# Kernel tuning notes

Hardware: AMD Instinct MI355X
Metric: run time of the kernel (lower is better)

Reference implementation:

```python
import jax, jax.numpy as jnp
import numpy as np

B, S, HID, NH = 2, 2048, 1024, 16
HD = HID // NH
BASE = 10000.0


def _rope_tables(seq_len, head_dim):
    i = jnp.arange(0, head_dim, 2, dtype=jnp.float32)
    theta = BASE ** (-i / head_dim)
    pos = jnp.arange(seq_len, dtype=jnp.float32)
    m_theta = jnp.outer(pos, theta)  # [S, HD/2]
    cos = jnp.repeat(jnp.cos(m_theta), 2, axis=1)  # [S, HD]
    sin = jnp.repeat(jnp.sin(m_theta), 2, axis=1)
    return cos, sin


def _apply_rope(x, cos, sin):
    # x: [B, NH, S, HD]; interleaved rotation: (-x1, x0, -x3, x2, ...)
    x_even = x[..., 0::2]
    x_odd = x[..., 1::2]
    inv_x = jnp.stack((-x_odd, x_even), axis=-1).reshape(x.shape)
    return x * cos[None, None] + inv_x * sin[None, None]


def setup_inputs() -> dict:
    key = jax.random.key(0)
    ks = jax.random.split(key, 7)
    q = jax.random.normal(ks[0], (B, S, HID), dtype=jnp.float32)
    k = jax.random.normal(ks[1], (B, S, HID), dtype=jnp.float32)
    v = jax.random.normal(ks[2], (B, S, HID), dtype=jnp.float32)
    scale = 1.0 / np.sqrt(HID)
    Wq = jax.random.normal(ks[3], (HID, HID), dtype=jnp.float32) * scale
    Wk = jax.random.normal(ks[4], (HID, HID), dtype=jnp.float32) * scale
    Wv = jax.random.normal(ks[5], (HID, HID), dtype=jnp.float32) * scale
    Wo = jax.random.normal(ks[6], (HID, HID), dtype=jnp.float32) * scale
    mask = jnp.triu(jnp.ones((S, S), dtype=bool), k=1)[None, None]  # causal, True = masked
    return {"q": q, "k": k, "v": v, "mask": mask,
            "Wq": Wq, "Wk": Wk, "Wv": Wv, "Wo": Wo}


def reference(q, k, v, mask, Wq, Wk, Wv, Wo):
    cos, sin = _rope_tables(S, HD)
    # Linear (torch stores weight as [out, in]; y = x @ W.T)
    qh = (q @ Wq.T).reshape(B, S, NH, HD).transpose(0, 2, 1, 3)
    kh = (k @ Wk.T).reshape(B, S, NH, HD).transpose(0, 2, 1, 3)
    vh = (v @ Wv.T).reshape(B, S, NH, HD).transpose(0, 2, 1, 3)
    qh = _apply_rope(qh, cos, sin)
    kh = _apply_rope(kh, cos, sin)
    scores = jnp.einsum("bhqd,bhkd->bhqk", qh, kh) / np.sqrt(HD)
    neg_min = jnp.finfo(jnp.float32).min
    scores = jnp.where(mask, neg_min, scores)
    attn = jax.nn.softmax(scores, axis=-1)
    out = jnp.einsum("bhqk,bhkd->bhqd", attn, vh)  # [B,NH,S,HD]
    out = out.transpose(0, 2, 1, 3).reshape(B, S, HID)
    return out @ Wo.T
```

## Files before the change

kernel.cpp:

```cpp
#include <hip/hip_runtime.h>

#define S_LEN 2048
#define HIDN  1024
#define NHEAD 16
#define HDIM  64
#define MROWS 4096
#define KDIM  1024
#define NDIM  1024

typedef __attribute__((ext_vector_type(8))) short bf16x8;
typedef __attribute__((ext_vector_type(4))) float f32x4;

static __device__ __forceinline__ ushort f2bf(float f) {
    unsigned int u = __float_as_uint(f);
    u = (u + 0x7fffu + ((u >> 16) & 1u)) >> 16;
    return (ushort)u;
}

static __device__ __forceinline__ void gload16(const ushort* g, ushort* l) {
    __builtin_amdgcn_global_load_lds(
        (const __attribute__((address_space(1))) unsigned int*)g,
        (__attribute__((address_space(3))) unsigned int*)l, 16, 0, 0);
}

__global__ __launch_bounds__(256) void prep_kernel(
    const float* __restrict__ q, const float* __restrict__ k,
    const float* __restrict__ v, const float* __restrict__ Wq,
    const float* __restrict__ Wk, const float* __restrict__ Wv,
    const float* __restrict__ Wo,
    ushort* __restrict__ qb, ushort* __restrict__ kb, ushort* __restrict__ vb,
    ushort* __restrict__ Wqb, ushort* __restrict__ Wkb, ushort* __restrict__ Wvb,
    ushort* __restrict__ Wob,
    float* __restrict__ rc, float* __restrict__ rs)
{
    const long Q4 = (long)MROWS * KDIM / 4;
    const long W4 = (long)NDIM * KDIM / 4;
    if (blockIdx.x < 16384) {
        long i = (long)blockIdx.x * 256 + threadIdx.x;
        const float* src; ushort* dst; long off;
        if (i < Q4)          { src = q; dst = qb; off = i; }
        else if (i < 2 * Q4) { src = k; dst = kb; off = i - Q4; }
        else if (i < 3 * Q4) { src = v; dst = vb; off = i - 2 * Q4; }
        else {
            long t = i - 3 * Q4;
            int wsel = (int)(t >> 18);
            off = t & (W4 - 1);
            src = (wsel == 0) ? Wq : (wsel == 1) ? Wk : (wsel == 2) ? Wv : Wo;
            dst = (wsel == 0) ? Wqb : (wsel == 1) ? Wkb : (wsel == 2) ? Wvb : Wob;
        }
        float4 vv = ((const float4*)src)[off];
        ushort4 o;
        o.x = f2bf(vv.x); o.y = f2bf(vv.y); o.z = f2bf(vv.z); o.w = f2bf(vv.w);
        ((ushort4*)dst)[off] = o;
    } else {
        int idx = (blockIdx.x - 16384) * 256 + threadIdx.x;
        int s  = idx >> 5;
        int jp = idx & 31;
        float theta = expf(-(float)(2 * jp) * (9.210340371976184f / 64.0f));
        float ang = (float)s * theta;
        float sv, cv;
        sincosf(ang, &sv, &cv);
        rc[idx] = cv;
        rs[idx] = sv;
    }
}

static __device__ __forceinline__ void gemm_mainloop(
    const ushort* __restrict__ A, const ushort* __restrict__ W,
    ushort* As, ushort* Bs, f32x4 (&acc)[4][4], bool swapops,
    int m0, int n0, int tid)
{
    const int lane = tid & 63, wid = tid >> 6;
    const int wm = wid & 1, wn = wid >> 1;
    const int quad = lane >> 4, l15 = lane & 15;

    for (int k0 = 0; k0 < KDIM; k0 += 32) {
        __syncthreads();
#pragma unroll
        for (int rr = 0; rr < 2; ++rr) {
            int sidx = tid + rr * 256;
            int row = sidx >> 2;
            int g = (sidx & 3) ^ (row & 3);
            gload16(A + (size_t)(m0 + row) * KDIM + k0 + g * 8, As + sidx * 8);
            gload16(W + (size_t)(n0 + row) * KDIM + k0 + g * 8, Bs + sidx * 8);
        }
        __syncthreads();

        bf16x8 af[4], bfr[4];
#pragma unroll
        for (int i = 0; i < 4; ++i) {
            int row = wm * 64 + i * 16 + l15;
            int p = quad ^ (row & 3);
            af[i] = swapops ? *(const bf16x8*)&Bs[row * 32 + p * 8]
                            : *(const bf16x8*)&As[row * 32 + p * 8];
        }
#pragma unroll
        for (int j = 0; j < 4; ++j) {
            int row = wn * 64 + j * 16 + l15;
            int p = quad ^ (row & 3);
            bfr[j] = swapops ? *(const bf16x8*)&As[row * 32 + p * 8]
                             : *(const bf16x8*)&Bs[row * 32 + p * 8];
        }
#pragma unroll
        for (int i = 0; i < 4; ++i)
#pragma unroll
            for (int j = 0; j < 4; ++j)
                acc[i][j] = __builtin_amdgcn_mfma_f32_16x16x32_bf16(af[i], bfr[j],
                                                                    acc[i][j], 0, 0, 0);
    }
}

__global__ __launch_bounds__(256) void gemm_qkv(
    const ushort* __restrict__ qb, const ushort* __restrict__ kb,
    const ushort* __restrict__ vb,
    const ushort* __restrict__ Wqb, const ushort* __restrict__ Wkb,
    const ushort* __restrict__ Wvb,
    ushort* __restrict__ Qh, ushort* __restrict__ Kh, ushort* __restrict__ Vt,
    const float* __restrict__ rc, const float* __restrict__ rs)
{
    __shared__ __align__(16) ushort As[128 * 32];
    __shared__ __align__(16) ushort Bs[128 * 32];

    const int tid = threadIdx.x;
    const int lane = tid & 63, wid = tid >> 6;
    const int wm = wid & 1, wn = wid >> 1;
    const int quad = lane >> 4, l15 = lane & 15;
    const int m0 = blockIdx.y * 128, n0 = blockIdx.x * 128;
    const int z = blockIdx.z;

    const ushort* A = (z == 0) ? qb : (z == 1) ? kb : vb;
    const ushort* W = (z == 0) ? Wqb : (z == 1) ? Wkb : Wvb;

    f32x4 acc[4][4];
#pragma unroll
    for (int i = 0; i < 4; ++i)
#pragma unroll
        for (int j = 0; j < 4; ++j) acc[i][j] = 0.0f;

    gemm_mainloop(A, W, As, Bs, acc, (z == 2), m0, n0, tid);

    if (z != 2) {
        ushort* out = (z == 0) ? Qh : Kh;
        const float scale = (z == 0) ? 0.18033688011112042f : 1.0f;
#pragma unroll
        for (int i = 0; i < 4; ++i)
#pragma unroll
            for (int j = 0; j < 4; ++j)
#pragma unroll
                for (int r = 0; r < 4; ++r) {
                    int m = m0 + wm * 64 + i * 16 + quad * 4 + r;
                    int n = n0 + wn * 64 + j * 16 + l15;
                    float v = acc[i][j][r];
                    int b = m >> 11, s = m & (S_LEN - 1);
                    int h = n >> 6, d = n & 63;
                    int pidx = s * 32 + (d >> 1);
                    float cv = rc[pidx], sv = rs[pidx];
                    float partner = __shfl_xor(v, 1);
                    v = (d & 1) ? (v * cv + partner * sv)
                                : (v * cv - partner * sv);
                    out[((size_t)((b * NHEAD + h) * S_LEN + s)) * HDIM + d] =
                        f2bf(v * scale);
                }
    } else {
#pragma unroll
        for (int i = 0; i < 4; ++i)
#pragma unroll
            for (int j = 0; j < 4; ++j)
#pragma unroll
                for (int r = 0; r < 4; ++r) {
                    int nrow = n0 + wm * 64 + i * 16 + quad * 4 + r;
                    int mcol = m0 + wn * 64 + j * 16 + l15;
                    int h = nrow >> 6, d = nrow & 63;
                    int b = mcol >> 11, s = mcol & (S_LEN - 1);
                    Vt[((size_t)((b * NHEAD + h) * HDIM + d)) * S_LEN + s] =
                        f2bf(acc[i][j][r]);
                }
    }
}

__global__ __launch_bounds__(256) void gemm_out(
    const ushort* __restrict__ A, const ushort* __restrict__ W,
    float* __restrict__ out)
{
    __shared__ __align__(16) ushort As[128 * 32];
    __shared__ __align__(16) ushort Bs[128 * 32];

    const int tid = threadIdx.x;
    const int lane = tid & 63, wid = tid >> 6;
    const int wm = wid & 1, wn = wid >> 1;
    const int quad = lane >> 4, l15 = lane & 15;
    const int m0 = blockIdx.y * 128, n0 = blockIdx.x * 128;

    f32x4 acc[4][4];
#pragma unroll
    for (int i = 0; i < 4; ++i)
#pragma unroll
        for (int j = 0; j < 4; ++j) acc[i][j] = 0.0f;

    gemm_mainloop(A, W, As, Bs, acc, false, m0, n0, tid);

#pragma unroll
    for (int i = 0; i < 4; ++i)
#pragma unroll
        for (int j = 0; j < 4; ++j)
#pragma unroll
            for (int r = 0; r < 4; ++r) {
                int m = m0 + wm * 64 + i * 16 + quad * 4 + r;
                int n = n0 + wn * 64 + j * 16 + l15;
                out[(size_t)m * NDIM + n] = acc[i][j][r];
            }
}

__global__ __launch_bounds__(256) void attn_mfma(
    const ushort* __restrict__ Qh, const ushort* __restrict__ Kh,
    const ushort* __restrict__ Vt, ushort* __restrict__ AO)
{
    __shared__ __align__(16) ushort Ks[64 * 64];
    __shared__ __align__(16) ushort Vs[64 * 64];
    __shared__ __align__(16) ushort Ps[64 * 72];

    const int tid = threadIdx.x;
    const int lane = tid & 63, w = tid >> 6;
    const int quad = lane >> 4, l15 = lane & 15;
    const int id = blockIdx.x;
    const int b = id >> 9, h = (id >> 5) & 15, xr = id & 31;
    const int qt = b ? (31 - xr) : xr;
    const int q0 = qt * 64;
    const size_t hoff = (size_t)(b * NHEAD + h) * S_LEN * HDIM;

    bf16x8 qf[2];
#pragma unroll
    for (int ks = 0; ks < 2; ++ks)
        qf[ks] = *(const bf16x8*)(Qh + hoff +
            (size_t)(q0 + w * 16 + l15) * HDIM + ks * 32 + quad * 8);

    bf16x8 ones;
#pragma unroll
    for (int i = 0; i < 8; ++i) ones[i] = (short)0x3F80;

    f32x4 Oa[4];
    f32x4 Lacc = 0.0f;
#pragma unroll
    for (int j = 0; j < 4; ++j) Oa[j] = 0.0f;

    const int rowq = q0 + w * 16 + quad * 4;

    for (int kt = 0; kt <= qt; ++kt) {
        const int k0 = kt * 64;
        const bool diag = (kt == qt);
        __syncthreads();
#pragma unroll
        for (int rr = 0; rr < 2; ++rr) {
            int sidx = tid + rr * 256;
            int row = sidx >> 3;
            int g = (sidx & 7) ^ (row & 7);
            gload16(Kh + hoff + (size_t)(k0 + row) * HDIM + g * 8, Ks + sidx * 8);
            gload16(Vt + hoff + (size_t)row * S_LEN + k0 + g * 8, Vs + sidx * 8);
        }
        __syncthreads();

        f32x4 Sa[4];
#pragma unroll
        for (int j = 0; j < 4; ++j) Sa[j] = 0.0f;
#pragma unroll
        for (int ks = 0; ks < 2; ++ks) {
            const int p = ((ks << 2) | quad) ^ (l15 & 7);
            bf16x8 kf[4];
#pragma unroll
            for (int j = 0; j < 4; ++j)
                kf[j] = *(const bf16x8*)&Ks[(j * 16 + l15) * 64 + p * 8];
#pragma unroll
            for (int j = 0; j < 4; ++j)
                Sa[j] = __builtin_amdgcn_mfma_f32_16x16x32_bf16(qf[ks], kf[j],
                                                                Sa[j], 0, 0, 0);
        }

#pragma unroll
        for (int j = 0; j < 4; ++j) {
#pragma unroll
            for (int r = 0; r < 4; ++r) {
                float p = exp2f(Sa[j][r]);
                if (diag) {
                    int key = k0 + j * 16 + l15;
                    if (key > rowq + r) p = 0.f;
                }
                Ps[(w * 16 + quad * 4 + r) * 72 + j * 16 + l15] =
                    (ushort)(__float_as_uint(p) >> 16);
            }
        }

#pragma unroll
        for (int ks = 0; ks < 2; ++ks) {
            const int p = ((ks << 2) | quad) ^ (l15 & 7);
            bf16x8 pf = *(const bf16x8*)&Ps[(w * 16 + l15) * 72 + ks * 32 + quad * 8];
            bf16x8 vf[4];
#pragma unroll
            for (int j = 0; j < 4; ++j)
                vf[j] = *(const bf16x8*)&Vs[(j * 16 + l15) * 64 + p * 8];
#pragma unroll
            for (int j = 0; j < 4; ++j)
                Oa[j] = __builtin_amdgcn_mfma_f32_16x16x32_bf16(pf, vf[j],
                                                                Oa[j], 0, 0, 0);
            Lacc = __builtin_amdgcn_mfma_f32_16x16x32_bf16(pf, ones, Lacc, 0, 0, 0);
        }
    }

#pragma unroll
    for (int r = 0; r < 4; ++r) {
        float inv = 1.0f / Lacc[r];
        int srow = rowq + r;
#pragma unroll
        for (int j = 0; j < 4; ++j) {
            int d = j * 16 + l15;
            AO[((size_t)(b * S_LEN + srow)) * HIDN + h * HDIM + d] =
                f2bf(Oa[j][r] * inv);
        }
    }
}

extern "C" void kernel_launch(void* const* d_in, const int* in_sizes, int n_in,
                              void* d_out, int out_size, void* d_ws, size_t ws_size,
                              hipStream_t stream) {
    const float* qf  = (const float*)d_in[0];
    const float* kf  = (const float*)d_in[1];
    const float* vf  = (const float*)d_in[2];
    const float* Wqf = (const float*)d_in[4];
    const float* Wkf = (const float*)d_in[5];
    const float* Wvf = (const float*)d_in[6];
    const float* Wof = (const float*)d_in[7];
    float* out = (float*)d_out;

    char* wsp = (char*)d_ws;
    float* rc = (float*)wsp;            wsp += 65536 * 4;
    float* rs = (float*)wsp;            wsp += 65536 * 4;
    ushort* qb  = (ushort*)wsp;         wsp += (size_t)MROWS * KDIM * 2;
    ushort* kb  = (ushort*)wsp;         wsp += (size_t)MROWS * KDIM * 2;
    ushort* vb  = (ushort*)wsp;         wsp += (size_t)MROWS * KDIM * 2;
    ushort* Wqb = (ushort*)wsp;         wsp += (size_t)NDIM * KDIM * 2;
    ushort* Wkb = (ushort*)wsp;         wsp += (size_t)NDIM * KDIM * 2;
    ushort* Wvb = (ushort*)wsp;         wsp += (size_t)NDIM * KDIM * 2;
    ushort* Wob = (ushort*)wsp;         wsp += (size_t)NDIM * KDIM * 2;
    ushort* Qh  = (ushort*)wsp;         wsp += (size_t)MROWS * HIDN * 2;
    ushort* Kh  = (ushort*)wsp;         wsp += (size_t)MROWS * HIDN * 2;
    ushort* Vt  = (ushort*)wsp;         wsp += (size_t)MROWS * HIDN * 2;
    ushort* AO  = (ushort*)wsp;

    prep_kernel<<<16640, 256, 0, stream>>>(qf, kf, vf, Wqf, Wkf, Wvf, Wof,
                                           qb, kb, vb, Wqb, Wkb, Wvb, Wob, rc, rs);

    gemm_qkv<<<dim3(NDIM / 128, MROWS / 128, 3), 256, 0, stream>>>(
        qb, kb, vb, Wqb, Wkb, Wvb, Qh, Kh, Vt, rc, rs);

    attn_mfma<<<1024, 256, 0, stream>>>(Qh, Kh, Vt, AO);

    gemm_out<<<dim3(NDIM / 128, MROWS / 128), 256, 0, stream>>>(AO, Wob, out);
}
```

Measured before the change: 243.6 us.

## Double GEMM K-tile to 64 and use 128-row query tiles in attention

The GEMM mainloop now stages 64-wide K slices in LDS with an 8-way XOR swizzle. This halves the number of barrier-separated iterations and doubles the MFMA work per sync. The attention kernel now gives each block 128 query rows, two 16-row subtiles per wave, so each K/V tile loaded into LDS is reused across twice as many queries. The trade-off is more registers and LDS per block and half as many attention blocks (512), which may reduce occupancy and load balance.

```diff
diff --git a/kernel.cpp b/kernel.cpp
--- a/kernel.cpp
+++ b/kernel.cpp
@@ -74,39 +74,42 @@
     const int wm = wid & 1, wn = wid >> 1;
     const int quad = lane >> 4, l15 = lane & 15;
 
-    for (int k0 = 0; k0 < KDIM; k0 += 32) {
+    for (int k0 = 0; k0 < KDIM; k0 += 64) {
         __syncthreads();
 #pragma unroll
-        for (int rr = 0; rr < 2; ++rr) {
+        for (int rr = 0; rr < 4; ++rr) {
             int sidx = tid + rr * 256;
-            int row = sidx >> 2;
-            int g = (sidx & 3) ^ (row & 3);
+            int row = sidx >> 3;
+            int g = (sidx & 7) ^ (row & 7);
             gload16(A + (size_t)(m0 + row) * KDIM + k0 + g * 8, As + sidx * 8);
             gload16(W + (size_t)(n0 + row) * KDIM + k0 + g * 8, Bs + sidx * 8);
         }
         __syncthreads();
 
-        bf16x8 af[4], bfr[4];
-#pragma unroll
-        for (int i = 0; i < 4; ++i) {
-            int row = wm * 64 + i * 16 + l15;
-            int p = quad ^ (row & 3);
-            af[i] = swapops ? *(const bf16x8*)&Bs[row * 32 + p * 8]
-                            : *(const bf16x8*)&As[row * 32 + p * 8];
-        }
-#pragma unroll
-        for (int j = 0; j < 4; ++j) {
-            int row = wn * 64 + j * 16 + l15;
-            int p = quad ^ (row & 3);
-            bfr[j] = swapops ? *(const bf16x8*)&As[row * 32 + p * 8]
-                             : *(const bf16x8*)&Bs[row * 32 + p * 8];
-        }
-#pragma unroll
-        for (int i = 0; i < 4; ++i)
-#pragma unroll
-            for (int j = 0; j < 4; ++j)
-                acc[i][j] = __builtin_amdgcn_mfma_f32_16x16x32_bf16(af[i], bfr[j],
-                                                                    acc[i][j], 0, 0, 0);
+#pragma unroll
+        for (int ks = 0; ks < 2; ++ks) {
+            bf16x8 af[4], bfr[4];
+#pragma unroll
+            for (int i = 0; i < 4; ++i) {
+                int row = wm * 64 + i * 16 + l15;
+                int gg = ((ks << 2) | quad) ^ (row & 7);
+                af[i] = swapops ? *(const bf16x8*)&Bs[row * 64 + gg * 8]
+                                : *(const bf16x8*)&As[row * 64 + gg * 8];
+            }
+#pragma unroll
+            for (int j = 0; j < 4; ++j) {
+                int row = wn * 64 + j * 16 + l15;
+                int gg = ((ks << 2) | quad) ^ (row & 7);
+                bfr[j] = swapops ? *(const bf16x8*)&As[row * 64 + gg * 8]
+                                 : *(const bf16x8*)&Bs[row * 64 + gg * 8];
+            }
+#pragma unroll
+            for (int i = 0; i < 4; ++i)
+#pragma unroll
+                for (int j = 0; j < 4; ++j)
+                    acc[i][j] = __builtin_amdgcn_mfma_f32_16x16x32_bf16(
+                        af[i], bfr[j], acc[i][j], 0, 0, 0);
+        }
     }
 }
 
@@ -118,8 +121,8 @@
     ushort* __restrict__ Qh, ushort* __restrict__ Kh, ushort* __restrict__ Vt,
     const float* __restrict__ rc, const float* __restrict__ rs)
 {
-    __shared__ __align__(16) ushort As[128 * 32];
-    __shared__ __align__(16) ushort Bs[128 * 32];
+    __shared__ __align__(16) ushort As[128 * 64];
+    __shared__ __align__(16) ushort Bs[128 * 64];
 
     const int tid = threadIdx.x;
     const int lane = tid & 63, wid = tid >> 6;
@@ -182,8 +185,8 @@
     const ushort* __restrict__ A, const ushort* __restrict__ W,
     float* __restrict__ out)
 {
-    __shared__ __align__(16) ushort As[128 * 32];
-    __shared__ __align__(16) ushort Bs[128 * 32];
+    __shared__ __align__(16) ushort As[128 * 64];
+    __shared__ __align__(16) ushort Bs[128 * 64];
 
     const int tid = threadIdx.x;
     const int lane = tid & 63, wid = tid >> 6;
@@ -217,37 +220,42 @@
 {
     __shared__ __align__(16) ushort Ks[64 * 64];
     __shared__ __align__(16) ushort Vs[64 * 64];
-    __shared__ __align__(16) ushort Ps[64 * 72];
+    __shared__ __align__(16) ushort Ps[128 * 72];
 
     const int tid = threadIdx.x;
     const int lane = tid & 63, w = tid >> 6;
     const int quad = lane >> 4, l15 = lane & 15;
     const int id = blockIdx.x;
-    const int b = id >> 9, h = (id >> 5) & 15, xr = id & 31;
-    const int qt = b ? (31 - xr) : xr;
-    const int q0 = qt * 64;
+    const int b = id >> 8, h = (id >> 4) & 15, xr = id & 15;
+    const int qt = b ? (15 - xr) : xr;
+    const int q0 = qt * 128;
     const size_t hoff = (size_t)(b * NHEAD + h) * S_LEN * HDIM;
 
-    bf16x8 qf[2];
-#pragma unroll
-    for (int ks = 0; ks < 2; ++ks)
-        qf[ks] = *(const bf16x8*)(Qh + hoff +
-            (size_t)(q0 + w * 16 + l15) * HDIM + ks * 32 + quad * 8);
+    bf16x8 qf[2][2];
+#pragma unroll
+    for (int i = 0; i < 2; ++i)
+#pragma unroll
+        for (int ks = 0; ks < 2; ++ks)
+            qf[i][ks] = *(const bf16x8*)(Qh + hoff +
+                (size_t)(q0 + w * 32 + i * 16 + l15) * HDIM + ks * 32 + quad * 8);
 
     bf16x8 ones;
 #pragma unroll
     for (int i = 0; i < 8; ++i) ones[i] = (short)0x3F80;
 
-    f32x4 Oa[4];
-    f32x4 Lacc = 0.0f;
-#pragma unroll
-    for (int j = 0; j < 4; ++j) Oa[j] = 0.0f;
-
-    const int rowq = q0 + w * 16 + quad * 4;
-
-    for (int kt = 0; kt <= qt; ++kt) {
+    f32x4 Oa[2][4];
+    f32x4 Lacc[2];
+#pragma unroll
+    for (int i = 0; i < 2; ++i) {
+        Lacc[i] = 0.0f;
+#pragma unroll
+        for (int j = 0; j < 4; ++j) Oa[i][j] = 0.0f;
+    }
+
+    const int nkt = 2 * qt + 2;
+    for (int kt = 0; kt < nkt; ++kt) {
         const int k0 = kt * 64;
-        const bool diag = (kt == qt);
+        const bool masked = (kt >= 2 * qt);
         __syncthreads();
 #pragma unroll
         for (int rr = 0; rr < 2; ++rr) {
@@ -259,9 +267,11 @@
         }
         __syncthreads();
 
-        f32x4 Sa[4];
-#pragma unroll
-        for (int j = 0; j < 4; ++j) Sa[j] = 0.0f;
+        f32x4 Sa[2][4];
+#pragma unroll
+        for (int i = 0; i < 2; ++i)
+#pragma unroll
+            for (int j = 0; j < 4; ++j) Sa[i][j] = 0.0f;
 #pragma unroll
         for (int ks = 0; ks < 2; ++ks) {
             const int p = ((ks << 2) | quad) ^ (l15 & 7);
@@ -270,52 +280,67 @@
             for (int j = 0; j < 4; ++j)
                 kf[j] = *(const bf16x8*)&Ks[(j * 16 + l15) * 64 + p * 8];
 #pragma unroll
-            for (int j = 0; j < 4; ++j)
-                Sa[j] = __builtin_amdgcn_mfma_f32_16x16x32_bf16(qf[ks], kf[j],
-                                                                Sa[j], 0, 0, 0);
-        }
-
-#pragma unroll
-        for (int j = 0; j < 4; ++j) {
-#pragma unroll
-            for (int r = 0; r < 4; ++r) {
-                float p = exp2f(Sa[j][r]);
-                if (diag) {
-                    int key = k0 + j * 16 + l15;
-                    if (key > rowq + r) p = 0.f;
+            for (int i = 0; i < 2; ++i)
+#pragma unroll
+                for (int j = 0; j < 4; ++j)
+                    Sa[i][j] = __builtin_amdgcn_mfma_f32_16x16x32_bf16(
+                        qf[i][ks], kf[j], Sa[i][j], 0, 0, 0);
+        }
+
+#pragma unroll
+        for (int i = 0; i < 2; ++i) {
+            const int rbase = q0 + w * 32 + i * 16 + quad * 4;
+#pragma unroll
+            for (int j = 0; j < 4; ++j) {
+#pragma unroll
+                for (int r = 0; r < 4; ++r) {
+                    float p = exp2f(Sa[i][j][r]);
+                    if (masked) {
+                        int key = k0 + j * 16 + l15;
+                        if (key > rbase + r) p = 0.f;
+                    }
+                    Ps[(w * 32 + i * 16 + quad * 4 + r) * 72 + j * 16 + l15] =
+                        (ushort)(__float_as_uint(p) >> 16);
                 }
-                Ps[(w * 16 + quad * 4 + r) * 72 + j * 16 + l15] =
-                    (ushort)(__float_as_uint(p) >> 16);
             }
         }
 
 #pragma unroll
         for (int ks = 0; ks < 2; ++ks) {
             const int p = ((ks << 2) | quad) ^ (l15 & 7);
-            bf16x8 pf = *(const bf16x8*)&Ps[(w * 16 + l15) * 72 + ks * 32 + quad * 8];
-            bf16x8 vf[4];
+            bf16x8 pf[2], vf[4];
+#pragma unroll
+            for (int i = 0; i < 2; ++i)
+                pf[i] = *(const bf16x8*)&Ps[(w * 32 + i * 16 + l15) * 72 +
+                                            ks * 32 + quad * 8];
 #pragma unroll
             for (int j = 0; j < 4; ++j)
                 vf[j] = *(const bf16x8*)&Vs[(j * 16 + l15) * 64 + p * 8];
 #pragma unroll
-            for (int j = 0; j < 4; ++j)
-                Oa[j] = __builtin_amdgcn_mfma_f32_16x16x32_bf16(pf, vf[j],
-                                                                Oa[j], 0, 0, 0);
-            Lacc = __builtin_amdgcn_mfma_f32_16x16x32_bf16(pf, ones, Lacc, 0, 0, 0);
-        }
-    }
-
-#pragma unroll
-    for (int r = 0; r < 4; ++r) {
-        float inv = 1.0f / Lacc[r];
-        int srow = rowq + r;
-#pragma unroll
-        for (int j = 0; j < 4; ++j) {
-            int d = j * 16 + l15;
-            AO[((size_t)(b * S_LEN + srow)) * HIDN + h * HDIM + d] =
-                f2bf(Oa[j][r] * inv);
-        }
-    }
+            for (int i = 0; i < 2; ++i) {
+#pragma unroll
+                for (int j = 0; j < 4; ++j)
+                    Oa[i][j] = __builtin_amdgcn_mfma_f32_16x16x32_bf16(
+                        pf[i], vf[j], Oa[i][j], 0, 0, 0);
+                Lacc[i] = __builtin_amdgcn_mfma_f32_16x16x32_bf16(
+                    pf[i], ones, Lacc[i], 0, 0, 0);
+            }
+        }
+    }
+
+#pragma unroll
+    for (int i = 0; i < 2; ++i)
+#pragma unroll
+        for (int r = 0; r < 4; ++r) {
+            float inv = 1.0f / Lacc[i][r];
+            int srow = q0 + w * 32 + i * 16 + quad * 4 + r;
+#pragma unroll
+            for (int j = 0; j < 4; ++j) {
+                int d = j * 16 + l15;
+                AO[((size_t)(b * S_LEN + srow)) * HIDN + h * HDIM + d] =
+                    f2bf(Oa[i][j][r] * inv);
+            }
+        }
 }
 
 extern "C" void kernel_launch(void* const* d_in, const int* in_sizes, int n_in,
@@ -351,7 +376,7 @@
     gemm_qkv<<<dim3(NDIM / 128, MROWS / 128, 3), 256, 0, stream>>>(
         qb, kb, vb, Wqb, Wkb, Wvb, Qh, Kh, Vt, rc, rs);
 
-    attn_mfma<<<1024, 256, 0, stream>>>(Qh, Kh, Vt, AO);
+    attn_mfma<<<512, 256, 0, stream>>>(Qh, Kh, Vt, AO);
 
     gemm_out<<<dim3(NDIM / 128, MROWS / 128), 256, 0, stream>>>(AO, Wob, out);
 }
```

New measurement: 247.5 us. No clear change (+1.6%).
